# Kernel tuning notes

Measured on AMD Instinct MI355X. Metric: run time of the kernel, lower is better.

Reference implementation:

```python
import jax, jax.numpy as jnp
import numpy as np

INF = 1e12  # constant.INFINITY_NUMBER in the original repo
NEG = -1e30  # stand-in for -inf in masked softmax (grad-safe)


def pool_max(h, mask):
    # h: [B,S,D], mask: [B,S,1] bool (True = masked out)
    return jnp.max(jnp.where(mask, -INF, h), axis=1)


def setup_inputs() -> dict:
    key = jax.random.key(0)
    B, S, V = 512, 128, 50000
    D_EMB, D_POS, D_NER, D_DEP = 300, 30, 30, 100
    HID = 300
    IN = D_EMB + D_POS + D_NER  # 360
    NPOS, NNER, NDEP, NCLS = 54, 23, 42, 42
    ks = jax.random.split(key, 16)
    words = jax.random.randint(ks[0], (B, S), 1, V)
    pos = jax.random.randint(ks[1], (B, S), 1, NPOS)
    ner = jax.random.randint(ks[2], (B, S), 1, NNER)
    deprel = jax.random.randint(ks[3], (B, S), 1, NDEP)
    # random dependency tree: head of token t is a random earlier token; token 0 is root
    rng = np.random.default_rng(0)
    heads = np.zeros((B, S), dtype=np.int64)
    for t in range(1, S):
        heads[:, t] = rng.integers(0, t, size=B)
    adj_np = np.zeros((B, S, S), dtype=np.float32)
    bi = np.arange(B)[:, None]
    ti = np.arange(1, S)[None, :]
    adj_np[bi, heads[:, 1:], np.broadcast_to(ti, (B, S - 1))] = 1.0  # directed head->dep, no self-loop
    adj = jnp.asarray(adj_np)
    # subj at position 5, obj at position 20 (subj_pos/obj_pos are relative offsets; ==0 marks entity)
    subj_pos = (jnp.broadcast_to(jnp.arange(S), (B, S)) - 5).astype(jnp.int32)
    obj_pos = (jnp.broadcast_to(jnp.arange(S), (B, S)) - 20).astype(jnp.int32)

    def p(k, shape, scale=0.02):
        return jax.random.normal(k, shape, jnp.float32) * scale

    return dict(
        words=words, pos=pos, ner=ner, deprel=deprel,
        subj_pos=subj_pos, obj_pos=obj_pos, adj=adj,
        emb_w=p(ks[4], (V, D_EMB)),
        pos_w=p(ks[5], (NPOS, D_POS)),
        ner_w=p(ks[6], (NNER, D_NER)),
        dep_w=p(ks[7], (NDEP, D_DEP)),
        attn_w=p(ks[8], (D_DEP, IN), 0.001),  # Attention.weight ~ N(0, 0.001)
        W0=p(ks[9], (IN, HID)), b0=jnp.zeros((HID,), jnp.float32),
        W1=p(ks[10], (HID, HID)), b1=jnp.zeros((HID,), jnp.float32),
        mlp0_w=p(ks[11], (3 * HID, HID)), mlp0_b=jnp.zeros((HID,), jnp.float32),
        mlp1_w=p(ks[12], (HID, HID)), mlp1_b=jnp.zeros((HID,), jnp.float32),
        cls_w=p(ks[13], (HID, NCLS)), cls_b=jnp.zeros((NCLS,), jnp.float32),
    )


def reference(words, pos, ner, deprel, subj_pos, obj_pos, adj,
              emb_w, pos_w, ner_w, dep_w, attn_w,
              W0, b0, W1, b1, mlp0_w, mlp0_b, mlp1_w, mlp1_b, cls_w, cls_b):
    # embeddings -> [B,S,360]
    h = jnp.concatenate([emb_w[words], pos_w[pos], ner_w[ner]], axis=2)
    denom = jnp.sum(adj, axis=2, keepdims=True) + 1.0  # [B,S,1]
    pool_mask = ((jnp.sum(adj, axis=2) + jnp.sum(adj, axis=1)) == 0)[:, :, None]  # [B,S,1]
    d_mask = jnp.sum(adj, axis=1) == 0  # [B,S] (in-degree zero)
    # deprel attention -> edge weights
    dep_e = jnp.where(d_mask[:, :, None], 0.0, dep_w[deprel])  # [B,S,Ddep]
    query = pool_max(h, pool_mask)  # [B,360]
    scores = jnp.einsum('bsd,de,be->bs', dep_e, attn_w, query)
    scores = jnp.where(d_mask, NEG, scores)
    weights = jax.nn.softmax(scores, axis=1)  # [B,S]
    a = adj * weights[:, :, None]
    a = a + jnp.swapaxes(a, 1, 2)  # symmetrize
    # GCN layers: AxW = W(Ax) + W(h) => (Ax+h)@W + 2b, degree-normalized, ReLU
    for W, b in ((W0, b0), (W1, b1)):
        Ax = jnp.einsum('bst,btd->bsd', a, h)
        h = jax.nn.relu(((Ax + h) @ W + 2.0 * b) / denom)
    subj_mask = (subj_pos != 0)[:, :, None]
    obj_mask = (obj_pos != 0)[:, :, None]
    h_out = pool_max(h, pool_mask)
    subj_out = pool_max(h, subj_mask)
    obj_out = pool_max(h, obj_mask)
    out = jnp.concatenate([h_out, subj_out, obj_out], axis=1)  # [B,900]
    out = jax.nn.relu(out @ mlp0_w + mlp0_b)
    out = jax.nn.relu(out @ mlp1_w + mlp1_b)
    logits = out @ cls_w + cls_b
    return logits, h_out
```

## Files before the change

### kernel.cpp

```cpp
#include <hip/hip_runtime.h>
#include <cstdint>

typedef __bf16 bf16;
typedef bf16 bf16x8 __attribute__((ext_vector_type(8)));
typedef float f32x4 __attribute__((ext_vector_type(4)));

#define NB 512
#define SS 128
#define DIN 360
#define DINP 384
#define DHID 300
#define DHP 320
#define DDEPW 100
#define NCLS 42
#define KCAT 928

constexpr float INF_ = 1e12f;
constexpr float NEG_ = -1e30f;

__global__ void k_degrees(const float* __restrict__ adj, float* __restrict__ denom,
                          int* __restrict__ pmask, int* __restrict__ dmask) {
  int b = blockIdx.x, t = threadIdx.x;
  const float* A = adj + (size_t)b * SS * SS;
  float indeg = 0.f;
  for (int s = 0; s < SS; ++s) indeg += A[s * SS + t];
  float outdeg = 0.f;
  const float4* row = (const float4*)(A + t * SS);
#pragma unroll
  for (int i = 0; i < SS / 4; ++i) { float4 v = row[i]; outdeg += v.x + v.y + v.z + v.w; }
  int idx = b * SS + t;
  denom[idx] = outdeg + 1.f;
  pmask[idx] = ((indeg + outdeg) == 0.f) ? 1 : 0;
  dmask[idx] = (indeg == 0.f) ? 1 : 0;
}

__global__ void k_embed(const int* __restrict__ words, const int* __restrict__ pos,
                        const int* __restrict__ ner,
                        const float* __restrict__ emb_w, const float* __restrict__ pos_w,
                        const float* __restrict__ ner_w, bf16* __restrict__ h) {
  int tid = threadIdx.x;
  int tok0 = blockIdx.x * 16;
  for (int i = 0; i < 16; ++i) {
    int tok = tok0 + i;
    if (tid < 180) {
      int c = tid * 2;
      float2 v;
      if (c < 300)      v = *(const float2*)(emb_w + (size_t)words[tok] * 300 + c);
      else if (c < 330) v = *(const float2*)(pos_w + (size_t)pos[tok] * 30 + (c - 300));
      else              v = *(const float2*)(ner_w + (size_t)ner[tok] * 30 + (c - 330));
      union { bf16 b[2]; uint32_t u; } cvt;
      cvt.b[0] = (bf16)v.x; cvt.b[1] = (bf16)v.y;
      *(uint32_t*)(h + (size_t)tok * DINP + c) = cvt.u;
    } else {
      int c = 360 + (tid - 180) * 2;
      *(uint32_t*)(h + (size_t)tok * DINP + c) = 0u;
    }
  }
}

__global__ void k_prepw(const float* __restrict__ W, int K, int N,
                        bf16* __restrict__ WT, int RP, int SP) {
  int idx = blockIdx.x * 256 + threadIdx.x;
  if (idx >= RP * SP) return;
  int r = idx / SP, c = idx % SP;
  float v = (r < N && c < K) ? W[(size_t)c * N + r] : 0.f;
  WT[(size_t)r * SP + c] = (bf16)v;
}

__global__ void k_prepwb(const float* __restrict__ W, int K, int N,
                         bf16* __restrict__ WT, int KP, int NP) {
  int idx = blockIdx.x * 256 + threadIdx.x;
  if (idx >= NP * KP) return;
  int n = idx / KP, k = idx - n * KP;
  float v = (n < N && k < K) ? W[(size_t)k * N + n] : 0.f;
  WT[(size_t)n * KP + k] = (bf16)v;
}

__global__ void k_query_qa(const bf16* __restrict__ h, const int* __restrict__ pmask,
                           const float* __restrict__ attn_w, float* __restrict__ qa) {
  __shared__ float q[DIN];
  __shared__ int pm[SS];
  int b = blockIdx.x, tid = threadIdx.x;
  if (tid < SS) pm[tid] = pmask[b * SS + tid];
  __syncthreads();
  if (tid < DIN) {
    float m = -INF_;
    const bf16* hb = h + (size_t)b * SS * DINP + tid;
    for (int s = 0; s < SS; ++s) { float v = (float)hb[(size_t)s * DINP]; if (!pm[s]) m = fmaxf(m, v); }
    q[tid] = m;
  }
  __syncthreads();
  if (tid < DDEPW) {
    const float* wr = attn_w + (size_t)tid * DIN;
    float acc = 0.f;
    for (int e = 0; e < DIN; ++e) acc += wr[e] * q[e];
    qa[b * SS + tid] = acc;
  }
}

__global__ void k_weights(const int* __restrict__ deprel, const float* __restrict__ dep_w,
                          const int* __restrict__ dmask, const float* __restrict__ qa,
                          float* __restrict__ wts) {
  __shared__ float qs[DDEPW];
  __shared__ float red[SS];
  int b = blockIdx.x, s = threadIdx.x;
  if (s < DDEPW) qs[s] = qa[b * SS + s];
  __syncthreads();
  float score;
  if (dmask[b * SS + s]) score = NEG_;
  else {
    const float* dr = dep_w + (size_t)deprel[b * SS + s] * DDEPW;
    float acc = 0.f;
    for (int d = 0; d < DDEPW; ++d) acc += dr[d] * qs[d];
    score = acc;
  }
  red[s] = score; __syncthreads();
  for (int off = 64; off > 0; off >>= 1) { if (s < off) red[s] = fmaxf(red[s], red[s + off]); __syncthreads(); }
  float mx = red[0]; __syncthreads();
  float ex = expf(score - mx);
  red[s] = ex; __syncthreads();
  for (int off = 64; off > 0; off >>= 1) { if (s < off) red[s] += red[s + off]; __syncthreads(); }
  wts[b * SS + s] = ex / red[0];
}

__global__ void k_symmetrize(const float* __restrict__ adj, const float* __restrict__ wts,
                             bf16* __restrict__ amat) {
  __shared__ float tile[SS * SS];
  int b = blockIdx.x, tid = threadIdx.x;
  const float* Ab = adj + (size_t)b * SS * SS;
  bf16* ab = amat + (size_t)b * SS * SS;
#pragma unroll 4
  for (int i = 0; i < 64; ++i) {
    int idx = i * 256 + tid;
    int s_ = idx >> 7, t_ = idx & 127;
    tile[(s_ << 7) + ((t_ + s_) & 127)] = Ab[idx];
  }
  __syncthreads();
  const float* wb = wts + b * SS;
#pragma unroll 4
  for (int i = 0; i < 64; ++i) {
    int idx = i * 256 + tid;
    int s_ = idx >> 7, t_ = idx & 127;
    float v = tile[(s_ << 7) + ((t_ + s_) & 127)] * wb[s_]
            + tile[(t_ << 7) + ((s_ + t_) & 127)] * wb[t_];
    ab[idx] = (bf16)v;
  }
}

__global__ __launch_bounds__(256) void k_ah(
    const bf16* __restrict__ amat, const bf16* __restrict__ h,
    int SH, int NVALID, bf16* __restrict__ t, int ST) {
  __shared__ __align__(16) bf16 Xs[128 * 136];
  __shared__ __align__(16) bf16 Ys[32 * 136];
  int z = blockIdx.y;
  int nblk = blockIdx.x * 128;
  int tid = threadIdx.x;
  const bf16* Az = amat + (size_t)z * SS * SS;
  const bf16* hz = h + (size_t)z * SS * SH;
  {
    int c8 = (tid & 15) * 8;
#pragma unroll
    for (int it = 0; it < 8; ++it) {
      int r = it * 16 + (tid >> 4);
      *(bf16x8*)&Xs[r * 136 + c8] = *(const bf16x8*)&Az[r * SS + c8];
    }
  }
  int wid = tid >> 6, lane = tid & 63;
  int wm = (wid >> 1) * 64, wn = (wid & 1) * 64;
  int lr = lane & 15, lg = lane >> 4;
  f32x4 acc[4][4];
#pragma unroll
  for (int i = 0; i < 4; ++i)
#pragma unroll
    for (int j = 0; j < 4; ++j) acc[i][j] = (f32x4){0.f, 0.f, 0.f, 0.f};

  for (int k0 = 0; k0 < SS; k0 += 32) {
    {
      int c8 = (tid & 15) * 8;
      int col = nblk + c8;
#pragma unroll
      for (int it = 0; it < 2; ++it) {
        int r = it * 16 + (tid >> 4);
        bf16x8 v;
        if (col < SH) v = *(const bf16x8*)&hz[(size_t)(k0 + r) * SH + col];
        else { union { uint32_t u[4]; bf16x8 bv; } zz; zz.u[0]=zz.u[1]=zz.u[2]=zz.u[3]=0u; v = zz.bv; }
        *(bf16x8*)&Ys[r * 136 + c8] = v;
      }
    }
    __syncthreads();
    bf16x8 a[4], b[4];
#pragma unroll
    for (int mi = 0; mi < 4; ++mi)
      a[mi] = *(const bf16x8*)&Xs[(wm + mi * 16 + lr) * 136 + k0 + lg * 8];
#pragma unroll
    for (int nf = 0; nf < 4; ++nf) {
      bf16x8 bv;
#pragma unroll
      for (int i = 0; i < 8; ++i) bv[i] = Ys[(lg * 8 + i) * 136 + wn + nf * 16 + lr];
      b[nf] = bv;
    }
#pragma unroll
    for (int mi = 0; mi < 4; ++mi)
#pragma unroll
      for (int nf = 0; nf < 4; ++nf)
        acc[mi][nf] = __builtin_amdgcn_mfma_f32_16x16x32_bf16(a[mi], b[nf], acc[mi][nf], 0, 0, 0);
    __syncthreads();
  }
#pragma unroll
  for (int mi = 0; mi < 4; ++mi) {
    int m = wm + mi * 16 + lg * 4;
#pragma unroll
    for (int nf = 0; nf < 4; ++nf) {
      int n = nblk + wn + nf * 16 + lr;
      if (n < ST) {
#pragma unroll
        for (int i = 0; i < 4; ++i) {
          float v = (n < NVALID) ? (acc[mi][nf][i] + (float)hz[(size_t)(m + i) * SH + n]) : 0.f;
          t[((size_t)z * SS + m + i) * ST + n] = (bf16)v;
        }
      }
    }
  }
}

template<bool F32OUT>
__global__ __launch_bounds__(256) void k_dense(
    const bf16* __restrict__ X, const bf16* __restrict__ Y,
    const float* __restrict__ bias, const float* __restrict__ denom,
    void* __restrict__ Cout, int K, int NVALID, int SC) {
  __shared__ __align__(16) bf16 As[128 * 40];
  __shared__ __align__(16) bf16 Bs[160 * 40];
  int tid = threadIdx.x;
  int mblk = blockIdx.y * 128, nblk = blockIdx.x * 160;
  int wid = tid >> 6, lane = tid & 63;
  int wm = (wid >> 1) * 64, wn = (wid & 1) * 80;
  int lr = lane & 15, lg = lane >> 4;
  f32x4 acc[4][5];
#pragma unroll
  for (int i = 0; i < 4; ++i)
#pragma unroll
    for (int j = 0; j < 5; ++j) acc[i][j] = (f32x4){0.f, 0.f, 0.f, 0.f};
  int rA = tid >> 2, kA = (tid & 3) * 8;
  for (int k0 = 0; k0 < K; k0 += 32) {
#pragma unroll
    for (int it = 0; it < 2; ++it) {
      int r = it * 64 + rA;
      *(bf16x8*)&As[r * 40 + kA] = *(const bf16x8*)&X[(size_t)(mblk + r) * K + k0 + kA];
    }
#pragma unroll
    for (int it = 0; it < 3; ++it) {
      int r = it * 64 + rA;
      if (r < 160)
        *(bf16x8*)&Bs[r * 40 + kA] = *(const bf16x8*)&Y[(size_t)(nblk + r) * K + k0 + kA];
    }
    __syncthreads();
    bf16x8 a[4], b[5];
#pragma unroll
    for (int mi = 0; mi < 4; ++mi)
      a[mi] = *(const bf16x8*)&As[(wm + mi * 16 + lr) * 40 + lg * 8];
#pragma unroll
    for (int nf = 0; nf < 5; ++nf)
      b[nf] = *(const bf16x8*)&Bs[(wn + nf * 16 + lr) * 40 + lg * 8];
#pragma unroll
    for (int mi = 0; mi < 4; ++mi)
#pragma unroll
      for (int nf = 0; nf < 5; ++nf)
        acc[mi][nf] = __builtin_amdgcn_mfma_f32_16x16x32_bf16(a[mi], b[nf], acc[mi][nf], 0, 0, 0);
    __syncthreads();
  }
#pragma unroll
  for (int mi = 0; mi < 4; ++mi) {
    int m0 = mblk + wm + mi * 16 + lg * 4;
    float dn[4];
#pragma unroll
    for (int i = 0; i < 4; ++i) dn[i] = denom[m0 + i];
#pragma unroll
    for (int nf = 0; nf < 5; ++nf) {
      int n = nblk + wn + nf * 16 + lr;
      if (n < NVALID) {
        float bs = 2.f * bias[n];
#pragma unroll
        for (int i = 0; i < 4; ++i) {
          float v = fmaxf((acc[mi][nf][i] + bs) / dn[i], 0.f);
          if (F32OUT) ((float*)Cout)[(size_t)(m0 + i) * SC + n] = v;
          else ((bf16*)Cout)[(size_t)(m0 + i) * SC + n] = (bf16)v;
        }
      }
    }
  }
}

template<bool RELU, bool BF16OUT, int KP, int NP, int NVALID>
__global__ __launch_bounds__(256) void k_mlp_mfma(
    const bf16* __restrict__ A, const bf16* __restrict__ BT,
    const float* __restrict__ bias, void* __restrict__ C, int M, int SC) {
  constexpr int NT = NP / 16;
  int wid = threadIdx.x >> 6, lane = threadIdx.x & 63;
  int wti = blockIdx.x * 4 + wid;
  int mt = wti / NT, nt = wti - mt * NT;
  if (mt * 16 >= M) return;
  int lr = lane & 15, lg = lane >> 4;
  const bf16* Ap = A + (size_t)(mt * 16 + lr) * KP + lg * 8;
  const bf16* Bp = BT + (size_t)(nt * 16 + lr) * KP + lg * 8;
  f32x4 acc = (f32x4){0.f, 0.f, 0.f, 0.f};
#pragma unroll
  for (int k0 = 0; k0 < KP; k0 += 32) {
    bf16x8 a = *(const bf16x8*)(Ap + k0);
    bf16x8 b = *(const bf16x8*)(Bp + k0);
    acc = __builtin_amdgcn_mfma_f32_16x16x32_bf16(a, b, acc, 0, 0, 0);
  }
  int n = nt * 16 + lr;
  int m0 = mt * 16 + lg * 4;
  float bs = (n < NVALID) ? bias[n] : 0.f;
  if (BF16OUT) {
#pragma unroll
    for (int i = 0; i < 4; ++i) {
      float v = 0.f;
      if (n < NVALID) { v = acc[i] + bs; if (RELU) v = fmaxf(v, 0.f); }
      ((bf16*)C)[(size_t)(m0 + i) * SC + n] = (bf16)v;
    }
  } else {
    if (n < NVALID) {
#pragma unroll
      for (int i = 0; i < 4; ++i) {
        float v = acc[i] + bs;
        if (RELU) v = fmaxf(v, 0.f);
        ((float*)C)[(size_t)(m0 + i) * SC + n] = v;
      }
    }
  }
}

__global__ void k_pool(const float* __restrict__ h, const int* __restrict__ pmask,
                       const int* __restrict__ subj_pos, const int* __restrict__ obj_pos,
                       bf16* __restrict__ catb, float* __restrict__ hout) {
  __shared__ int pm[SS], sm[SS], om[SS];
  int b = blockIdx.x, e = threadIdx.x;
  if (e < SS) {
    pm[e] = pmask[b * SS + e];
    sm[e] = (subj_pos[b * SS + e] != 0) ? 1 : 0;
    om[e] = (obj_pos[b * SS + e] != 0) ? 1 : 0;
  }
  __syncthreads();
  if (e < DHID) {
    const float* hb = h + (size_t)b * SS * DHID + e;
    float mh = -INF_, ms = -INF_, mo = -INF_;
    for (int s = 0; s < SS; ++s) {
      float v = hb[(size_t)s * DHID];
      if (!pm[s]) mh = fmaxf(mh, v);
      if (!sm[s]) ms = fmaxf(ms, v);
      if (!om[s]) mo = fmaxf(mo, v);
    }
    catb[(size_t)b * KCAT + e] = (bf16)mh;
    catb[(size_t)b * KCAT + 300 + e] = (bf16)ms;
    catb[(size_t)b * KCAT + 600 + e] = (bf16)mo;
    hout[(size_t)b * DHID + e] = mh;
  } else if (e < DHID + (KCAT - 3 * DHID)) {
    catb[(size_t)b * KCAT + 600 + e] = (bf16)0.f;
  }
}

extern "C" void kernel_launch(void* const* d_in, const int* in_sizes, int n_in,
                              void* d_out, int out_size, void* d_ws, size_t ws_size,
                              hipStream_t stream) {
  const int* words = (const int*)d_in[0];
  const int* pos = (const int*)d_in[1];
  const int* ner = (const int*)d_in[2];
  const int* deprel = (const int*)d_in[3];
  const int* subj_pos = (const int*)d_in[4];
  const int* obj_pos = (const int*)d_in[5];
  const float* adj = (const float*)d_in[6];
  const float* emb_w = (const float*)d_in[7];
  const float* pos_w = (const float*)d_in[8];
  const float* ner_w = (const float*)d_in[9];
  const float* dep_w = (const float*)d_in[10];
  const float* attn_w = (const float*)d_in[11];
  const float* W0 = (const float*)d_in[12];
  const float* b0 = (const float*)d_in[13];
  const float* W1 = (const float*)d_in[14];
  const float* b1 = (const float*)d_in[15];
  const float* mlp0_w = (const float*)d_in[16];
  const float* mlp0_b = (const float*)d_in[17];
  const float* mlp1_w = (const float*)d_in[18];
  const float* mlp1_b = (const float*)d_in[19];
  const float* cls_w = (const float*)d_in[20];
  const float* cls_b = (const float*)d_in[21];
  float* out = (float*)d_out;

  char* w = (char*)d_ws;
  bf16* h0 = (bf16*)w;
  bf16* h1 = (bf16*)w;
  float* h2f = (float*)w;
  w += 78643200;
  bf16* t1 = (bf16*)w;
  bf16* t2 = (bf16*)w;
  w += 50331648;
  bf16* amat = (bf16*)w; w += 16777216;
  bf16* W0T = (bf16*)w; w += 294912;
  bf16* W1T = (bf16*)w; w += 204800;
  float* denom = (float*)w; w += 262144;
  int* pmask = (int*)w; w += 262144;
  int* dmask = (int*)w; w += 262144;
  float* qa = (float*)w; w += 262144;
  float* wts = (float*)w; w += 262144;
  bf16* catb = (bf16*)w; w += 950272;
  bf16* m0b = (bf16*)w; w += 327680;
  bf16* m1b = (bf16*)w; w += 327680;
  bf16* M0T = (bf16*)w; w += 593920;
  bf16* M1T = (bf16*)w; w += 204800;
  bf16* CLT = (bf16*)w; w += 30720;

  k_prepw<<<(384 * 384 + 255) / 256, 256, 0, stream>>>(W0, DIN, DHID, W0T, DINP, DINP);
  k_prepw<<<(320 * 320 + 255) / 256, 256, 0, stream>>>(W1, DHID, DHID, W1T, DHP, DHP);
  k_prepwb<<<(320 * 928 + 255) / 256, 256, 0, stream>>>(mlp0_w, 900, DHID, M0T, KCAT, DHP);
  k_prepwb<<<(320 * 320 + 255) / 256, 256, 0, stream>>>(mlp1_w, DHID, DHID, M1T, DHP, DHP);
  k_prepwb<<<(48 * 320 + 255) / 256, 256, 0, stream>>>(cls_w, DHID, NCLS, CLT, DHP, 48);
  k_degrees<<<NB, SS, 0, stream>>>(adj, denom, pmask, dmask);
  k_embed<<<(NB * SS) / 16, 192, 0, stream>>>(words, pos, ner, emb_w, pos_w, ner_w, h0);
  k_query_qa<<<NB, 384, 0, stream>>>(h0, pmask, attn_w, qa);
  k_weights<<<NB, SS, 0, stream>>>(deprel, dep_w, dmask, qa, wts);
  k_symmetrize<<<NB, 256, 0, stream>>>(adj, wts, amat);

  k_ah<<<dim3(3, NB), 256, 0, stream>>>(amat, h0, DINP, DINP, t1, DINP);
  k_dense<false><<<dim3(2, NB), 256, 0, stream>>>(t1, W0T, b0, denom, h1, DINP, DHID, DHP);
  k_ah<<<dim3(3, NB), 256, 0, stream>>>(amat, h1, DHP, DHID, t2, DHP);
  k_dense<true><<<dim3(2, NB), 256, 0, stream>>>(t2, W1T, b1, denom, h2f, DHP, DHID, DHID);

  k_pool<<<NB, 384, 0, stream>>>(h2f, pmask, subj_pos, obj_pos, catb, out + NB * NCLS);

  k_mlp_mfma<true, true, KCAT, DHP, DHID><<<(512 / 16) * (DHP / 16) / 4, 256, 0, stream>>>(
      catb, M0T, mlp0_b, m0b, NB, DHP);
  k_mlp_mfma<true, true, DHP, DHP, DHID><<<(512 / 16) * (DHP / 16) / 4, 256, 0, stream>>>(
      m0b, M1T, mlp1_b, m1b, NB, DHP);
  k_mlp_mfma<false, false, DHP, 48, NCLS><<<(512 / 16) * (48 / 16) / 4, 256, 0, stream>>>(
      m1b, CLT, cls_b, out, NB, NCLS);
}
```

Baseline: 505.1 us.

## Use direct global-to-LDS loads with XOR swizzle and K=64 tiles in dense GEMM

The dense GEMM kernel now stages its A and B tiles with global_load_lds, which writes global memory straight into LDS and skips the register round trip. Each K step doubles from 32 to 64, and the LDS layout uses an XOR swizzle on 16-byte groups so fragment reads avoid bank conflicts. Launch bounds now request 4 blocks per CU. In exchange, LDS use per block grows, K must be a multiple of 64, and correctness depends on the swizzle mapping matching the wave-ordered LDS destination addresses.

```diff
diff --git a/kernel.cpp b/kernel.cpp
--- a/kernel.cpp
+++ b/kernel.cpp
@@ -17,6 +17,11 @@
 
 constexpr float INF_ = 1e12f;
 constexpr float NEG_ = -1e30f;
+
+__device__ __forceinline__ void gload16(const void* g, void* l) {
+  __builtin_amdgcn_global_load_lds((const __attribute__((address_space(1))) void*)g,
+                                   (__attribute__((address_space(3))) void*)l, 16, 0, 0);
+}
 
 __global__ void k_degrees(const float* __restrict__ adj, float* __restrict__ denom,
                           int* __restrict__ pmask, int* __restrict__ dmask) {
@@ -224,49 +229,58 @@
 }
 
 template<bool F32OUT>
-__global__ __launch_bounds__(256) void k_dense(
+__global__ __launch_bounds__(256, 4) void k_dense(
     const bf16* __restrict__ X, const bf16* __restrict__ Y,
     const float* __restrict__ bias, const float* __restrict__ denom,
     void* __restrict__ Cout, int K, int NVALID, int SC) {
-  __shared__ __align__(16) bf16 As[128 * 40];
-  __shared__ __align__(16) bf16 Bs[160 * 40];
+  __shared__ __align__(16) bf16 As[128 * 64];
+  __shared__ __align__(16) bf16 Bs[160 * 64];
   int tid = threadIdx.x;
   int mblk = blockIdx.y * 128, nblk = blockIdx.x * 160;
   int wid = tid >> 6, lane = tid & 63;
   int wm = (wid >> 1) * 64, wn = (wid & 1) * 80;
   int lr = lane & 15, lg = lane >> 4;
+  int srow = tid >> 3, slot = tid & 7;
   f32x4 acc[4][5];
 #pragma unroll
   for (int i = 0; i < 4; ++i)
 #pragma unroll
     for (int j = 0; j < 5; ++j) acc[i][j] = (f32x4){0.f, 0.f, 0.f, 0.f};
-  int rA = tid >> 2, kA = (tid & 3) * 8;
-  for (int k0 = 0; k0 < K; k0 += 32) {
-#pragma unroll
-    for (int it = 0; it < 2; ++it) {
-      int r = it * 64 + rA;
-      *(bf16x8*)&As[r * 40 + kA] = *(const bf16x8*)&X[(size_t)(mblk + r) * K + k0 + kA];
-    }
-#pragma unroll
-    for (int it = 0; it < 3; ++it) {
-      int r = it * 64 + rA;
-      if (r < 160)
-        *(bf16x8*)&Bs[r * 40 + kA] = *(const bf16x8*)&Y[(size_t)(nblk + r) * K + k0 + kA];
-    }
+
+  for (int k0 = 0; k0 < K; k0 += 64) {
     __syncthreads();
-    bf16x8 a[4], b[5];
-#pragma unroll
-    for (int mi = 0; mi < 4; ++mi)
-      a[mi] = *(const bf16x8*)&As[(wm + mi * 16 + lr) * 40 + lg * 8];
-#pragma unroll
-    for (int nf = 0; nf < 5; ++nf)
-      b[nf] = *(const bf16x8*)&Bs[(wn + nf * 16 + lr) * 40 + lg * 8];
-#pragma unroll
-    for (int mi = 0; mi < 4; ++mi)
-#pragma unroll
-      for (int nf = 0; nf < 5; ++nf)
-        acc[mi][nf] = __builtin_amdgcn_mfma_f32_16x16x32_bf16(a[mi], b[nf], acc[mi][nf], 0, 0, 0);
+#pragma unroll
+    for (int it = 0; it < 4; ++it) {
+      int row = it * 32 + srow;
+      int kg = slot ^ (row & 7);
+      gload16(&X[(size_t)(mblk + row) * K + k0 + kg * 8], &As[(it * 256 + wid * 64) * 8]);
+    }
+#pragma unroll
+    for (int it = 0; it < 5; ++it) {
+      int row = it * 32 + srow;
+      int kg = slot ^ (row & 7);
+      gload16(&Y[(size_t)(nblk + row) * K + k0 + kg * 8], &Bs[(it * 256 + wid * 64) * 8]);
+    }
     __syncthreads();
+#pragma unroll
+    for (int kk = 0; kk < 2; ++kk) {
+      bf16x8 a[4], b[5];
+#pragma unroll
+      for (int mi = 0; mi < 4; ++mi) {
+        int r = wm + mi * 16 + lr;
+        a[mi] = *(const bf16x8*)&As[r * 64 + (((kk * 4 + lg) ^ (lr & 7)) * 8)];
+      }
+#pragma unroll
+      for (int nf = 0; nf < 5; ++nf) {
+        int r = wn + nf * 16 + lr;
+        b[nf] = *(const bf16x8*)&Bs[r * 64 + (((kk * 4 + lg) ^ (lr & 7)) * 8)];
+      }
+#pragma unroll
+      for (int mi = 0; mi < 4; ++mi)
+#pragma unroll
+        for (int nf = 0; nf < 5; ++nf)
+          acc[mi][nf] = __builtin_amdgcn_mfma_f32_16x16x32_bf16(a[mi], b[nf], acc[mi][nf], 0, 0, 0);
+    }
   }
 #pragma unroll
   for (int mi = 0; mi < 4; ++mi) {
```

Measured after the change: 469.7 us. 7.0% less time.
